# Kernel tuning notes

Measured on AMD Instinct MI355X. Metric: run time of the kernel, lower is better.

The kernel has to match this reference:

```python
import jax, jax.numpy as jnp
import numpy as np

B, T, D, H, DFF = 64, 100, 1024, 16, 4096
HD = D // H
EPS = 1e-5


def _rope_tables(t_len, hd, dtype):
    # matches RotaryEmbedding: inv_freq over even dims, emb = cat([freqs, freqs])
    inv_freq = 1.0 / (10000.0 ** (jnp.arange(0, hd, 2, dtype=jnp.float32) / hd))
    t = jnp.arange(t_len, dtype=jnp.float32)
    freqs = jnp.einsum('i,j->ij', t, inv_freq)          # (T, hd/2)
    emb = jnp.concatenate([freqs, freqs], axis=-1)      # (T, hd)
    # apply_rope uses cos[..., ::2] / sin[..., ::2]
    cos = jnp.cos(emb)[:, ::2].astype(dtype)            # (T, hd/2)
    sin = jnp.sin(emb)[:, ::2].astype(dtype)
    return cos, sin


def _apply_rope(x, cos, sin):
    # x: (B, H, T, hd); cos/sin: (T, hd/2) broadcast over B,H
    x1 = x[..., ::2]
    x2 = x[..., 1::2]
    return jnp.concatenate([x1 * cos - x2 * sin, x1 * sin + x2 * cos], axis=-1)


def _layernorm(x, g, b):
    mu = jnp.mean(x, axis=-1, keepdims=True)
    var = jnp.mean(jnp.square(x - mu), axis=-1, keepdims=True)
    return (x - mu) * jax.lax.rsqrt(var + EPS) * g + b


def setup_inputs() -> dict:
    key = jax.random.key(0)
    ks = jax.random.split(key, 8)
    s = 0.02
    return {
        'tgt': jax.random.normal(ks[0], (B, T, D), dtype=jnp.float32),
        'Wqkv': jax.random.normal(ks[1], (3 * D, D), dtype=jnp.float32) * s,
        'bqkv': jnp.zeros((3 * D,), jnp.float32),
        'Wo': jax.random.normal(ks[2], (D, D), dtype=jnp.float32) * s,
        'bo': jnp.zeros((D,), jnp.float32),
        'W1': jax.random.normal(ks[3], (DFF, D), dtype=jnp.float32) * s,
        'b1': jnp.zeros((DFF,), jnp.float32),
        'W2': jax.random.normal(ks[4], (D, DFF), dtype=jnp.float32) * s,
        'b2': jnp.zeros((D,), jnp.float32),
        'g1': jnp.ones((D,), jnp.float32),
        'be1': jnp.zeros((D,), jnp.float32),
        'g2': jnp.ones((D,), jnp.float32),
        'be2': jnp.zeros((D,), jnp.float32),
        'tgt_mask': jnp.tril(jnp.ones((T, T), jnp.int32)),
    }


def reference(tgt, Wqkv, bqkv, Wo, bo, W1, b1, W2, b2, g1, be1, g2, be2, tgt_mask):
    dtype = tgt.dtype
    # QKV projection (torch Linear: x @ W.T + b)
    qkv = jnp.einsum('btd,ed->bte', tgt, Wqkv) + bqkv          # (B,T,3D)
    qkv = qkv.reshape(B, T, 3, H, HD).transpose(2, 0, 3, 1, 4)  # (3,B,H,T,hd)
    q, k, v = qkv[0], qkv[1], qkv[2]

    cos, sin = _rope_tables(T, HD, dtype)
    q = _apply_rope(q, cos, sin)
    k = _apply_rope(k, cos, sin)

    scale = 1.0 / np.sqrt(HD)
    scores = jnp.einsum('bhqd,bhkd->bhqk', q, k) * scale        # (B,H,T,T)
    scores = jnp.where(tgt_mask == 0, -jnp.inf, scores)
    attn = jax.nn.softmax(scores, axis=-1)
    ctx = jnp.einsum('bhqk,bhkd->bhqd', attn, v)                # (B,H,T,hd)
    ctx = ctx.transpose(0, 2, 1, 3).reshape(B, T, D)

    tgt2 = jnp.einsum('btd,ed->bte', ctx, Wo) + bo
    x = _layernorm(tgt + tgt2, g1, be1)

    h = jax.nn.relu(jnp.einsum('btd,fd->btf', x, W1) + b1)
    ff = jnp.einsum('btf,df->btd', h, W2) + b2
    out = _layernorm(x + ff, g2, be2)
    return out
```

## Files before the change

kernel.cpp:

```cpp
#include <hip/hip_runtime.h>
#include <math.h>

#define Bn   64
#define Tn   100
#define Tp   128
#define Dn   1024
#define Hn   16
#define HDn  64
#define DFFn 4096
#define EPSf 1e-5f

typedef unsigned short ushort_t;
typedef __attribute__((ext_vector_type(8))) __bf16 bf16x8;
typedef __attribute__((ext_vector_type(4))) float f32x4;

__device__ __forceinline__ float u2f(ushort_t u) {
    union { unsigned int i; float f; } v; v.i = ((unsigned int)u) << 16; return v.f;
}
__device__ __forceinline__ ushort_t f2bf(float f) {
    union { float f; unsigned int u; } v; v.f = f;
    unsigned int r = v.u + 0x7FFFu + ((v.u >> 16) & 1u);
    return (ushort_t)(r >> 16);
}

__device__ __forceinline__ void gload_lds16(const void* g, void* l) {
    __builtin_amdgcn_global_load_lds(
        (const __attribute__((address_space(1))) unsigned int*)g,
        (__attribute__((address_space(3))) unsigned int*)l,
        16, 0, 0);
}

#define VMWAIT_(n) asm volatile("s_waitcnt vmcnt(" #n ")" ::: "memory")
#define VMWAIT(n)  VMWAIT_(n)

struct ConvSeg { const float* src; ushort_t* dst; int n4; };
struct Conv5   { ConvSeg seg[5]; float2* tab; };

__global__ __launch_bounds__(256) void conv_bf16_multi(Conv5 cfg)
{
    if (blockIdx.x == gridDim.x - 1) {
        for (int e = threadIdx.x; e < Tn * 16; e += 256) {
            const int t = e >> 4, f = e & 15;
            float s, c;
            sincosf((float)t * exp2f(-0.83048202f * (float)f), &s, &c);
            cfg.tab[e] = make_float2(c, s);
        }
        return;
    }
    int i = blockIdx.x * 256 + threadIdx.x;
    #pragma unroll
    for (int s = 0; s < 5; ++s) {
        const int n = cfg.seg[s].n4;
        if (i < n) {
            float4 v = ((const float4*)cfg.seg[s].src)[i];
            ushort4 o;
            o.x = f2bf(v.x); o.y = f2bf(v.y); o.z = f2bf(v.z); o.w = f2bf(v.w);
            ((ushort4*)cfg.seg[s].dst)[i] = o;
            return;
        }
        i -= n;
    }
}

#define GEMM_TILE_MAP(gx_, gy_, swz_)                                        \
    const int L  = blockIdx.x;                                               \
    int rowt, colt;                                                          \
    if (swz_) {                                                              \
        const int group = L / (8 * (gx_));                                   \
        int l = L - group * 8 * (gx_);                                       \
        const int rem = (gy_) - group * 8;                                   \
        if (rem >= 8) { rowt = group * 8 + (l & 7); colt = l >> 3; }         \
        else          { rowt = group * 8 + l % rem; colt = l / rem; }        \
    } else { rowt = L / (gx_); colt = L - rowt * (gx_); }

template<bool RELU, bool ADDRES, typename OutT>
__global__ __launch_bounds__(256, 2) void gemm128_2p(const ushort_t* __restrict__ A,
                                                     const ushort_t* __restrict__ Bm,
                                                     const float* __restrict__ bias,
                                                     const ushort_t* __restrict__ res,
                                                     OutT* __restrict__ C,
                                                     int M, int N, int K,
                                                     int gx, int swz)
{
    __shared__ __align__(16) ushort_t As[2][128 * 64];
    __shared__ __align__(16) ushort_t Bs[2][128 * 64];

    const int gy = M >> 7;
    GEMM_TILE_MAP(gx, gy, swz)

    const int tid  = threadIdx.x;
    const int lane = tid & 63;
    const int wave = tid >> 6;
    const int wrow = (wave >> 1) * 64;
    const int wcol = (wave & 1) * 64;
    const int row0 = rowt * 128;
    const int col0 = colt * 128;
    const int frow = lane & 15;
    const int g    = lane >> 4;

    auto stage = [&](const ushort_t* src, int rowbase, ushort_t* lds) {
        #pragma unroll
        for (int i = 0; i < 4; ++i) {
            const int idx = i * 256 + tid;
            const int row = idx >> 3;
            const int gc  = (idx & 7) ^ (row & 7);
            gload_lds16(src + (size_t)(rowbase + row) * K + gc * 8, lds + idx * 8);
        }
    };

    f32x4 acc[4][4] = {};

    const int NT = K >> 6;
    stage(Bm,      col0, &Bs[0][0]);
    stage(A,       row0, &As[0][0]);
    stage(Bm + 64, col0, &Bs[1][0]);
    VMWAIT(4);
    __builtin_amdgcn_s_barrier();

    for (int t = 0; t < NT; ++t) {
        const int  buf = t & 1;
        const bool stA = (t + 1 < NT);
        const bool stB = (t + 2 < NT);

        bf16x8 bfr[4][2];
        #pragma unroll
        for (int j = 0; j < 4; ++j)
            #pragma unroll
            for (int kk = 0; kk < 2; ++kk) {
                const int rb = wcol + j * 16 + frow;
                const int ch = kk * 4 + g;
                bfr[j][kk] = *(const bf16x8*)&Bs[buf][rb * 64 + (ch ^ (rb & 7)) * 8];
            }
        bf16x8 af0[2][2];
        #pragma unroll
        for (int m = 0; m < 2; ++m)
            #pragma unroll
            for (int kk = 0; kk < 2; ++kk) {
                const int ra = wrow + m * 16 + frow;
                const int ch = kk * 4 + g;
                af0[m][kk] = *(const bf16x8*)&As[buf][ra * 64 + (ch ^ (ra & 7)) * 8];
            }
        if (stA) stage(A + (t + 1) * 64, row0, &As[buf ^ 1][0]);
        __builtin_amdgcn_s_barrier();
        asm volatile("s_waitcnt lgkmcnt(0)" ::: "memory");
        __builtin_amdgcn_sched_barrier(0);
        __builtin_amdgcn_s_setprio(1);
        #pragma unroll
        for (int m = 0; m < 2; ++m)
            #pragma unroll
            for (int j = 0; j < 4; ++j)
                #pragma unroll
                for (int kk = 0; kk < 2; ++kk)
                    acc[m][j] = __builtin_amdgcn_mfma_f32_16x16x32_bf16(
                        af0[m][kk], bfr[j][kk], acc[m][j], 0, 0, 0);
        __builtin_amdgcn_s_setprio(0);
        __builtin_amdgcn_sched_barrier(0);
        __builtin_amdgcn_s_barrier();

        bf16x8 af1[2][2];
        #pragma unroll
        for (int m = 0; m < 2; ++m)
            #pragma unroll
            for (int kk = 0; kk < 2; ++kk) {
                const int ra = wrow + (2 + m) * 16 + frow;
                const int ch = kk * 4 + g;
                af1[m][kk] = *(const bf16x8*)&As[buf][ra * 64 + (ch ^ (ra & 7)) * 8];
            }
        if (stB) stage(Bm + (t + 2) * 64, col0, &Bs[buf][0]);
        __builtin_amdgcn_s_barrier();
        asm volatile("s_waitcnt lgkmcnt(0)" ::: "memory");
        __builtin_amdgcn_sched_barrier(0);
        __builtin_amdgcn_s_setprio(1);
        #pragma unroll
        for (int m = 0; m < 2; ++m)
            #pragma unroll
            for (int j = 0; j < 4; ++j)
                #pragma unroll
                for (int kk = 0; kk < 2; ++kk)
                    acc[2 + m][j] = __builtin_amdgcn_mfma_f32_16x16x32_bf16(
                        af1[m][kk], bfr[j][kk], acc[2 + m][j], 0, 0, 0);
        __builtin_amdgcn_s_setprio(0);
        __builtin_amdgcn_sched_barrier(0);
        if (stB)      { VMWAIT(4); }
        else if (stA) { VMWAIT(0); }
        __builtin_amdgcn_s_barrier();
    }

    const int crow = (lane >> 4) * 4;
    const int ccol = lane & 15;
    #pragma unroll
    for (int i = 0; i < 4; ++i) {
        #pragma unroll
        for (int r = 0; r < 4; ++r) {
            const int row = row0 + wrow + i * 16 + crow + r;
            #pragma unroll
            for (int j = 0; j < 4; ++j) {
                const int col = col0 + wcol + j * 16 + ccol;
                float v = acc[i][j][r] + bias[col];
                if constexpr (ADDRES) v += u2f(res[(size_t)row * N + col]);
                if constexpr (RELU) v = fmaxf(v, 0.f);
                if constexpr (sizeof(OutT) == 2)
                    C[(size_t)row * N + col] = (OutT)f2bf(v);
                else
                    C[(size_t)row * N + col] = (OutT)v;
            }
        }
    }
}

__global__ __launch_bounds__(256) void rope_split(const ushort_t* __restrict__ qkv,
                                                  const float2*  __restrict__ tab,
                                                  ushort_t* __restrict__ q,
                                                  ushort_t* __restrict__ k,
                                                  ushort_t* __restrict__ vt)
{
    __shared__ ushort_t vls[64 * 130];

    const int bh  = blockIdx.x;
    const int b   = bh >> 4, h = bh & 15;
    const int tid = threadIdx.x;
    const size_t rowbase = (size_t)b * Tn * (3 * Dn) + h * HDn;

    const ushort_t* vsrc = qkv + rowbase + 2 * Dn;
    for (int idx = tid; idx < Tn * 64; idx += 256) {
        const int t = idx >> 6, d = idx & 63;
        vls[d * 130 + t] = vsrc[(size_t)t * (3 * Dn) + d];
    }

    #pragma unroll
    for (int s = 0; s < 2; ++s) {
        const ushort_t* src = qkv + rowbase + s * Dn;
        ushort_t* dst = (s ? k : q) + (size_t)bh * Tp * HDn;
        for (int idx = tid; idx < Tn * 32; idx += 256) {
            const int t = idx >> 5, p = idx & 31;
            const unsigned int xi =
                *(const unsigned int*)&src[(size_t)t * (3 * Dn) + 2 * p];
            const float x1 = u2f((ushort_t)(xi & 0xffffu));
            const float x2 = u2f((ushort_t)(xi >> 16));
            const float2 cs = tab[t * 16 + (p & 15)];
            dst[t * 64 + p]      = f2bf(x1 * cs.x - x2 * cs.y);
            dst[t * 64 + 32 + p] = f2bf(x1 * cs.y + x2 * cs.x);
        }
    }

    __syncthreads();

    ushort_t* vdst = vt + (size_t)bh * HDn * Tp;
    for (int idx = tid; idx < 64 * 64; idx += 256) {
        const int d  = idx >> 6;
        const int tt = (idx & 63) * 2;
        ushort2 o;
        o.x = (tt     < Tn) ? vls[d * 130 + tt]     : (ushort_t)0;
        o.y = (tt + 1 < Tn) ? vls[d * 130 + tt + 1] : (ushort_t)0;
        *(ushort2*)&vdst[d * Tp + tt] = o;
    }
}

__global__ __launch_bounds__(256) void attn_mfma(const ushort_t* __restrict__ q,
                                                 const ushort_t* __restrict__ k,
                                                 const ushort_t* __restrict__ vt,
                                                 ushort_t* __restrict__ ctx)
{
    __shared__ __align__(16) ushort_t sm[24576];

    const int bh   = blockIdx.x;
    const int b    = bh >> 4, h = bh & 15;
    const int tid  = threadIdx.x;
    const int wave = tid >> 6;
    const int lane = tid & 63;
    const int c    = lane & 15;
    const int g    = lane >> 4;
    const int R0   = wave * 32;

    const ushort_t* qg = q  + (size_t)bh * Tp * HDn;
    const ushort_t* kg = k  + (size_t)bh * Tp * HDn;
    const ushort_t* vg = vt + (size_t)bh * HDn * Tp;
    for (int s = wave; s < 16; s += 4) {
        const int idx = s * 64 + lane;
        { const int row = idx >> 3, pc = idx & 7, gc = pc ^ (row & 7);
          gload_lds16(qg + row * 64 + gc * 8, &sm[idx * 8]);
          gload_lds16(kg + row * 64 + gc * 8, &sm[8192 + idx * 8]); }
        { const int row = idx >> 4, pc = idx & 15, gc = pc ^ (row & 15);
          gload_lds16(vg + row * 128 + gc * 8, &sm[16384 + idx * 8]); }
    }
    __syncthreads();

    f32x4 acc[2][8] = {};
    #pragma unroll
    for (int ks = 0; ks < 2; ++ks) {
        const int cb = ks * 4;
        bf16x8 aq[2];
        #pragma unroll
        for (int i = 0; i < 2; ++i) {
            const int row = R0 + i * 16 + c;
            const int ph  = (cb + g) ^ (row & 7);
            aq[i] = *(const bf16x8*)&sm[row * 64 + ph * 8];
        }
        #pragma unroll
        for (int j = 0; j < 8; ++j) {
            const int row = j * 16 + c;
            const int ph  = (cb + g) ^ (row & 7);
            const bf16x8 bk = *(const bf16x8*)&sm[8192 + row * 64 + ph * 8];
            acc[0][j] = __builtin_amdgcn_mfma_f32_16x16x32_bf16(aq[0], bk, acc[0][j], 0, 0, 0);
            acc[1][j] = __builtin_amdgcn_mfma_f32_16x16x32_bf16(aq[1], bk, acc[1][j], 0, 0, 0);
        }
    }
    __syncthreads();

    float linv[2][4];
    #pragma unroll
    for (int i = 0; i < 2; ++i) {
        #pragma unroll
        for (int r = 0; r < 4; ++r) {
            const int row = R0 + i * 16 + g * 4 + r;
            float sv[8], m = -1e30f;
            #pragma unroll
            for (int j = 0; j < 8; ++j) {
                const int col = j * 16 + c;
                const float s = acc[i][j][r] * 0.125f;
                sv[j] = (col <= row) ? s : -1e30f;
                m = fmaxf(m, sv[j]);
            }
            #pragma unroll
            for (int msk = 1; msk < 16; msk <<= 1) m = fmaxf(m, __shfl_xor(m, msk));
            float l = 0.f;
            #pragma unroll
            for (int j = 0; j < 8; ++j) {
                const int col = j * 16 + c;
                const float p = (col <= row) ? __expf(sv[j] - m) : 0.f;
                sv[j] = p; l += p;
            }
            #pragma unroll
            for (int msk = 1; msk < 16; msk <<= 1) l += __shfl_xor(l, msk);
            linv[i][r] = 1.f / l;
            #pragma unroll
            for (int j = 0; j < 8; ++j) {
                const int chunk = j * 2 + (c >> 3);
                const int ph    = chunk ^ (row & 15);
                sm[row * 128 + ph * 8 + (c & 7)] = f2bf(sv[j]);
            }
        }
    }
    __syncthreads();

    f32x4 acc2[2][4] = {};
    #pragma unroll
    for (int ks = 0; ks < 4; ++ks) {
        const int cb = ks * 4;
        bf16x8 ap[2];
        #pragma unroll
        for (int i = 0; i < 2; ++i) {
            const int row = R0 + i * 16 + c;
            const int ph  = (cb + g) ^ (row & 15);
            ap[i] = *(const bf16x8*)&sm[row * 128 + ph * 8];
        }
        #pragma unroll
        for (int n = 0; n < 4; ++n) {
            const int row = n * 16 + c;
            const int ph  = (cb + g) ^ (row & 15);
            const bf16x8 bv = *(const bf16x8*)&sm[16384 + row * 128 + ph * 8];
            acc2[0][n] = __builtin_amdgcn_mfma_f32_16x16x32_bf16(ap[0], bv, acc2[0][n], 0, 0, 0);
            acc2[1][n] = __builtin_amdgcn_mfma_f32_16x16x32_bf16(ap[1], bv, acc2[1][n], 0, 0, 0);
        }
    }

    #pragma unroll
    for (int i = 0; i < 2; ++i) {
        #pragma unroll
        for (int r = 0; r < 4; ++r) {
            const int row = R0 + i * 16 + g * 4 + r;
            if (row < Tn) {
                const float s = linv[i][r];
                #pragma unroll
                for (int n = 0; n < 4; ++n) {
                    const int col = n * 16 + c;
                    ctx[(size_t)(b * Tn + row) * Dn + h * HDn + col] =
                        f2bf(acc2[i][n][r] * s);
                }
            }
        }
    }
}

__global__ __launch_bounds__(256) void ln_single(const ushort_t* __restrict__ a,
                                                 const float* __restrict__ g,
                                                 const float* __restrict__ be,
                                                 ushort_t* __restrict__ out_bf)
{
    const int row = blockIdx.x;
    const int tid = threadIdx.x;
    __shared__ float red[256];
    const size_t base = (size_t)row * Dn;

    float vals[4];
    float s = 0.f;
    #pragma unroll
    for (int i = 0; i < 4; ++i) {
        const int c = tid + i * 256;
        vals[i] = u2f(a[base + c]);
        s += vals[i];
    }
    red[tid] = s;
    __syncthreads();
    for (int o = 128; o > 0; o >>= 1) {
        if (tid < o) red[tid] += red[tid + o];
        __syncthreads();
    }
    const float mu = red[0] * (1.f / Dn);
    __syncthreads();

    float vs = 0.f;
    #pragma unroll
    for (int i = 0; i < 4; ++i) { const float d = vals[i] - mu; vs += d * d; }
    red[tid] = vs;
    __syncthreads();
    for (int o = 128; o > 0; o >>= 1) {
        if (tid < o) red[tid] += red[tid + o];
        __syncthreads();
    }
    const float rstd = rsqrtf(red[0] * (1.f / Dn) + EPSf);

    #pragma unroll
    for (int i = 0; i < 4; ++i) {
        const int c = tid + i * 256;
        out_bf[base + c] = f2bf((vals[i] - mu) * rstd * g[c] + be[c]);
    }
}

__global__ __launch_bounds__(256) void add_ln2(const ushort_t* __restrict__ a,
                                               const ushort_t* __restrict__ r,
                                               const float* __restrict__ g,
                                               const float* __restrict__ be,
                                               float* __restrict__ out)
{
    const int row = blockIdx.x;
    const int tid = threadIdx.x;
    __shared__ float red[256];
    const size_t base = (size_t)row * Dn;

    float vals[4];
    float s = 0.f;
    #pragma unroll
    for (int i = 0; i < 4; ++i) {
        const int c = tid + i * 256;
        vals[i] = u2f(a[base + c]) + u2f(r[base + c]);
        s += vals[i];
    }
    red[tid] = s;
    __syncthreads();
    for (int o = 128; o > 0; o >>= 1) {
        if (tid < o) red[tid] += red[tid + o];
        __syncthreads();
    }
    const float mu = red[0] * (1.f / Dn);
    __syncthreads();

    float vs = 0.f;
    #pragma unroll
    for (int i = 0; i < 4; ++i) { const float d = vals[i] - mu; vs += d * d; }
    red[tid] = vs;
    __syncthreads();
    for (int o = 128; o > 0; o >>= 1) {
        if (tid < o) red[tid] += red[tid + o];
        __syncthreads();
    }
    const float rstd = rsqrtf(red[0] * (1.f / Dn) + EPSf);

    #pragma unroll
    for (int i = 0; i < 4; ++i) {
        const int c = tid + i * 256;
        out[base + c] = (vals[i] - mu) * rstd * g[c] + be[c];
    }
}

extern "C" void kernel_launch(void* const* d_in, const int* in_sizes, int n_in,
                              void* d_out, int out_size, void* d_ws, size_t ws_size,
                              hipStream_t stream)
{
    const float* tgt  = (const float*)d_in[0];
    const float* Wqkv = (const float*)d_in[1];
    const float* bqkv = (const float*)d_in[2];
    const float* Wo   = (const float*)d_in[3];
    const float* bo   = (const float*)d_in[4];
    const float* W1   = (const float*)d_in[5];
    const float* b1   = (const float*)d_in[6];
    const float* W2   = (const float*)d_in[7];
    const float* b2   = (const float*)d_in[8];
    const float* g1   = (const float*)d_in[9];
    const float* be1  = (const float*)d_in[10];
    const float* g2   = (const float*)d_in[11];
    const float* be2  = (const float*)d_in[12];
    float* out = (float*)d_out;
    (void)in_sizes; (void)n_in; (void)out_size; (void)ws_size;

    const int M = Bn * Tn;

    char* w = (char*)d_ws;
    ushort_t* tgt_bf  = (ushort_t*)(w);
    ushort_t* Wqkv_bf = (ushort_t*)(w + 13107200);
    ushort_t* Wo_bf   = (ushort_t*)(w + 19398656);
    ushort_t* W1_bf   = (ushort_t*)(w + 21495808);
    ushort_t* W2_bf   = (ushort_t*)(w + 29884416);

    ushort_t* qb    = (ushort_t*)(w + 38273024);
    ushort_t* kb    = (ushort_t*)(w + 55050240);
    ushort_t* vtb   = (ushort_t*)(w + 71827456);
    ushort_t* hbuf  = (ushort_t*)(w + 38273024);
    ushort_t* qkvb  = (ushort_t*)(w + 88604672);
    ushort_t* ctxb  = (ushort_t*)(w + 88604672);
    ushort_t* tgt2b = (ushort_t*)(w + 101711872);
    ushort_t* ffb   = (ushort_t*)(w + 101711872);
    ushort_t* x_bf  = (ushort_t*)(w + 114819072);
    float2*   ropetab = (float2*)(w + 127926272);

    Conv5 cfg;
    cfg.seg[0] = { tgt,  tgt_bf,  M * Dn / 4 };
    cfg.seg[1] = { Wqkv, Wqkv_bf, 3 * Dn * Dn / 4 };
    cfg.seg[2] = { Wo,   Wo_bf,   Dn * Dn / 4 };
    cfg.seg[3] = { W1,   W1_bf,   DFFn * Dn / 4 };
    cfg.seg[4] = { W2,   W2_bf,   Dn * DFFn / 4 };
    cfg.tab    = ropetab;
    const int total4 = (M * Dn + 3 * Dn * Dn + Dn * Dn + 2 * DFFn * Dn) / 4;
    conv_bf16_multi<<<(total4 + 255) / 256 + 1, 256, 0, stream>>>(cfg);

    gemm128_2p<false, false, ushort_t><<<(M / 128) * (3 * Dn / 128), 256, 0, stream>>>(
        tgt_bf, Wqkv_bf, bqkv, nullptr, qkvb, M, 3 * Dn, Dn, 3 * Dn / 128, 1);
    rope_split<<<Bn * Hn, 256, 0, stream>>>(qkvb, ropetab, qb, kb, vtb);
    attn_mfma<<<Bn * Hn, 256, 0, stream>>>(qb, kb, vtb, ctxb);
    gemm128_2p<false, true, ushort_t><<<(M / 128) * (Dn / 128), 256, 0, stream>>>(
        ctxb, Wo_bf, bo, tgt_bf, tgt2b, M, Dn, Dn, Dn / 128, 1);
    ln_single<<<M, 256, 0, stream>>>(tgt2b, g1, be1, x_bf);
    gemm128_2p<true, false, ushort_t><<<(M / 128) * (DFFn / 128), 256, 0, stream>>>(
        x_bf, W1_bf, b1, nullptr, hbuf, M, DFFn, Dn, DFFn / 128, 0);
    gemm128_2p<false, false, ushort_t><<<(M / 128) * (Dn / 128), 256, 0, stream>>>(
        hbuf, W2_bf, b2, nullptr, ffb, M, Dn, DFFn, Dn / 128, 1);
    add_ln2<<<M, 256, 0, stream>>>(x_bf, ffb, g2, be2, out);
}
```

Measured before the change: 403.1 us.

## Collapse GEMM two-phase k-loop into single phase with triple-buffered B tiles

Restructures the bf16 MFMA GEMM main loop so each k-step loads all A and B fragments at once and issues all 32 MFMAs in a single phase, instead of two half-phases split by barriers. B tiles move to a 3-deep LDS ring so the prefetch of tile t+2 can be issued at the same point as the A prefetch. This removes one pair of barriers and one lgkm wait per k-step. In exchange it raises LDS use (80 KB per block), which may limit occupancy to two blocks per CU or fewer, and it raises register pressure from holding all A fragments at once.

```diff
diff --git a/kernel.cpp b/kernel.cpp
--- a/kernel.cpp
+++ b/kernel.cpp
@@ -74,7 +74,7 @@
     } else { rowt = L / (gx_); colt = L - rowt * (gx_); }
 
 template<bool RELU, bool ADDRES, typename OutT>
-__global__ __launch_bounds__(256, 2) void gemm128_2p(const ushort_t* __restrict__ A,
+__global__ __launch_bounds__(256, 2) void gemm128_1p(const ushort_t* __restrict__ A,
                                                      const ushort_t* __restrict__ Bm,
                                                      const float* __restrict__ bias,
                                                      const ushort_t* __restrict__ res,
@@ -83,7 +83,7 @@
                                                      int gx, int swz)
 {
     __shared__ __align__(16) ushort_t As[2][128 * 64];
-    __shared__ __align__(16) ushort_t Bs[2][128 * 64];
+    __shared__ __align__(16) ushort_t Bs[3][128 * 64];
 
     const int gy = M >> 7;
     GEMM_TILE_MAP(gx, gy, swz)
@@ -111,74 +111,49 @@
     f32x4 acc[4][4] = {};
 
     const int NT = K >> 6;
-    stage(Bm,      col0, &Bs[0][0]);
-    stage(A,       row0, &As[0][0]);
-    stage(Bm + 64, col0, &Bs[1][0]);
-    VMWAIT(4);
+    stage(Bm, col0, &Bs[0][0]);
+    stage(A,  row0, &As[0][0]);
+    if (NT > 1) { stage(Bm + 64, col0, &Bs[1][0]); VMWAIT(4); }
+    else        { VMWAIT(0); }
     __builtin_amdgcn_s_barrier();
 
     for (int t = 0; t < NT; ++t) {
-        const int  buf = t & 1;
-        const bool stA = (t + 1 < NT);
-        const bool stB = (t + 2 < NT);
-
-        bf16x8 bfr[4][2];
+        const int  bufA = t & 1;
+        const int  bufB = t % 3;
+        const bool stA  = (t + 1 < NT);
+        const bool stB  = (t + 2 < NT);
+
+        bf16x8 bfr[4][2], af[4][2];
         #pragma unroll
         for (int j = 0; j < 4; ++j)
             #pragma unroll
             for (int kk = 0; kk < 2; ++kk) {
                 const int rb = wcol + j * 16 + frow;
                 const int ch = kk * 4 + g;
-                bfr[j][kk] = *(const bf16x8*)&Bs[buf][rb * 64 + (ch ^ (rb & 7)) * 8];
-            }
-        bf16x8 af0[2][2];
-        #pragma unroll
-        for (int m = 0; m < 2; ++m)
+                bfr[j][kk] = *(const bf16x8*)&Bs[bufB][rb * 64 + (ch ^ (rb & 7)) * 8];
+            }
+        #pragma unroll
+        for (int m = 0; m < 4; ++m)
             #pragma unroll
             for (int kk = 0; kk < 2; ++kk) {
                 const int ra = wrow + m * 16 + frow;
                 const int ch = kk * 4 + g;
-                af0[m][kk] = *(const bf16x8*)&As[buf][ra * 64 + (ch ^ (ra & 7)) * 8];
-            }
-        if (stA) stage(A + (t + 1) * 64, row0, &As[buf ^ 1][0]);
+                af[m][kk] = *(const bf16x8*)&As[bufA][ra * 64 + (ch ^ (ra & 7)) * 8];
+            }
+        if (stA) stage(A + (t + 1) * 64,  row0, &As[bufA ^ 1][0]);
+        if (stB) stage(Bm + (t + 2) * 64, col0, &Bs[(t + 2) % 3][0]);
         __builtin_amdgcn_s_barrier();
         asm volatile("s_waitcnt lgkmcnt(0)" ::: "memory");
         __builtin_amdgcn_sched_barrier(0);
         __builtin_amdgcn_s_setprio(1);
         #pragma unroll
-        for (int m = 0; m < 2; ++m)
+        for (int m = 0; m < 4; ++m)
             #pragma unroll
             for (int j = 0; j < 4; ++j)
                 #pragma unroll
                 for (int kk = 0; kk < 2; ++kk)
                     acc[m][j] = __builtin_amdgcn_mfma_f32_16x16x32_bf16(
-                        af0[m][kk], bfr[j][kk], acc[m][j], 0, 0, 0);
-        __builtin_amdgcn_s_setprio(0);
-        __builtin_amdgcn_sched_barrier(0);
-        __builtin_amdgcn_s_barrier();
-
-        bf16x8 af1[2][2];
-        #pragma unroll
-        for (int m = 0; m < 2; ++m)
-            #pragma unroll
-            for (int kk = 0; kk < 2; ++kk) {
-                const int ra = wrow + (2 + m) * 16 + frow;
-                const int ch = kk * 4 + g;
-                af1[m][kk] = *(const bf16x8*)&As[buf][ra * 64 + (ch ^ (ra & 7)) * 8];
-            }
-        if (stB) stage(Bm + (t + 2) * 64, col0, &Bs[buf][0]);
-        __builtin_amdgcn_s_barrier();
-        asm volatile("s_waitcnt lgkmcnt(0)" ::: "memory");
-        __builtin_amdgcn_sched_barrier(0);
-        __builtin_amdgcn_s_setprio(1);
-        #pragma unroll
-        for (int m = 0; m < 2; ++m)
-            #pragma unroll
-            for (int j = 0; j < 4; ++j)
-                #pragma unroll
-                for (int kk = 0; kk < 2; ++kk)
-                    acc[2 + m][j] = __builtin_amdgcn_mfma_f32_16x16x32_bf16(
-                        af1[m][kk], bfr[j][kk], acc[2 + m][j], 0, 0, 0);
+                        af[m][kk], bfr[j][kk], acc[m][j], 0, 0, 0);
         __builtin_amdgcn_s_setprio(0);
         __builtin_amdgcn_sched_barrier(0);
         if (stB)      { VMWAIT(4); }
@@ -523,16 +498,16 @@
     const int total4 = (M * Dn + 3 * Dn * Dn + Dn * Dn + 2 * DFFn * Dn) / 4;
     conv_bf16_multi<<<(total4 + 255) / 256 + 1, 256, 0, stream>>>(cfg);
 
-    gemm128_2p<false, false, ushort_t><<<(M / 128) * (3 * Dn / 128), 256, 0, stream>>>(
+    gemm128_1p<false, false, ushort_t><<<(M / 128) * (3 * Dn / 128), 256, 0, stream>>>(
         tgt_bf, Wqkv_bf, bqkv, nullptr, qkvb, M, 3 * Dn, Dn, 3 * Dn / 128, 1);
     rope_split<<<Bn * Hn, 256, 0, stream>>>(qkvb, ropetab, qb, kb, vtb);
     attn_mfma<<<Bn * Hn, 256, 0, stream>>>(qb, kb, vtb, ctxb);
-    gemm128_2p<false, true, ushort_t><<<(M / 128) * (Dn / 128), 256, 0, stream>>>(
+    gemm128_1p<false, true, ushort_t><<<(M / 128) * (Dn / 128), 256, 0, stream>>>(
         ctxb, Wo_bf, bo, tgt_bf, tgt2b, M, Dn, Dn, Dn / 128, 1);
     ln_single<<<M, 256, 0, stream>>>(tgt2b, g1, be1, x_bf);
-    gemm128_2p<true, false, ushort_t><<<(M / 128) * (DFFn / 128), 256, 0, stream>>>(
+    gemm128_1p<true, false, ushort_t><<<(M / 128) * (DFFn / 128), 256, 0, stream>>>(
         x_bf, W1_bf, b1, nullptr, hbuf, M, DFFn, Dn, DFFn / 128, 0);
-    gemm128_2p<false, false, ushort_t><<<(M / 128) * (Dn / 128), 256, 0, stream>>>(
+    gemm128_1p<false, false, ushort_t><<<(M / 128) * (Dn / 128), 256, 0, stream>>>(
         hbuf, W2_bf, b2, nullptr, ffb, M, Dn, DFFn, Dn / 128, 1);
     add_ln2<<<M, 256, 0, stream>>>(x_bf, ffb, g2, be2, out);
 }
```

Measured after the change: 373.0 us. 1.08x faster.
